# Performance work log

Measured on AMD Instinct MI355X. Metric: run time of the kernel, lower is better.

The kernel has to match this reference:

```python
import jax, jax.numpy as jnp
import numpy as np

N, D, H, C, E, I, L, B = 16000, 128, 2, 128, 256000, 512, 2, 64
NTYPES = 10


def setup_inputs() -> dict:
    key = jax.random.key(0)
    ks = jax.random.split(key, 20)
    s = 0.05
    inp = {
        'x': jax.random.normal(ks[0], (N, D), jnp.float32),
        'hetro_emb': jax.random.normal(ks[1], (NTYPES, D), jnp.float32) * s,
        'Wq': jax.random.normal(ks[2], (D, H * C), jnp.float32) * s,
        'bq': jnp.zeros((H * C,), jnp.float32),
        'Wk': jax.random.normal(ks[3], (D, H * C), jnp.float32) * s,
        'bk': jnp.zeros((H * C,), jnp.float32),
        'Wv': jax.random.normal(ks[4], (D, H * C), jnp.float32) * s,
        'bv': jnp.zeros((H * C,), jnp.float32),
        'We': jax.random.normal(ks[5], (D, H * C), jnp.float32) * s,
        'Wskip': jax.random.normal(ks[6], (D, C), jnp.float32) * s,
        'bskip': jnp.zeros((C,), jnp.float32),
        'ln_gamma': jnp.ones((L, D), jnp.float32),
        'ln_beta': jnp.zeros((L, D), jnp.float32),
        'ffn_w1': jax.random.normal(ks[7], (L, D, I), jnp.float32) * s,
        'ffn_b1': jnp.zeros((L, I), jnp.float32),
        'ffn_w2': jax.random.normal(ks[8], (L, I, D), jnp.float32) * s,
        'ffn_b2': jnp.zeros((L, D), jnp.float32),
        'edge_index': jax.random.randint(ks[9], (2, E), 0, N, jnp.int64),
        'edge_type': jax.random.randint(ks[10], (E,), 0, NTYPES, jnp.int64),
        'mask_idx': jax.random.randint(ks[11], (B,), 0, N, jnp.int64),
    }
    return inp


def _layer_norm(h, gamma, beta, eps=1e-6):
    mu = h.mean(-1, keepdims=True)
    var = ((h - mu) ** 2).mean(-1, keepdims=True)
    return (h - mu) * jax.lax.rsqrt(var + eps) * gamma + beta


def reference(x, hetro_emb, Wq, bq, Wk, bk, Wv, bv, We, Wskip, bskip,
              ln_gamma, ln_beta, ffn_w1, ffn_b1, ffn_w2, ffn_b2,
              edge_index, edge_type, mask_idx):
    src, dst = edge_index[0], edge_index[1]  # messages flow src(j) -> dst(i)
    edge_attr_raw = hetro_emb[edge_type]     # [E, D], computed once outside the layer loop
    scale = 1.0 / jnp.sqrt(jnp.asarray(C, x.dtype))

    h = x
    pre = h
    for l in range(L):
        # shared GRANConv weights across layers (same module appended n_gcn_layer times)
        q = (h @ Wq + bq).reshape(-1, H, C)
        k = (h @ Wk + bk).reshape(-1, H, C)
        v = (h @ Wv + bv).reshape(-1, H, C)
        eproj = (edge_attr_raw @ We).reshape(-1, H, C)  # [E, H, C]
        kj = k[src] + eproj                              # [E, H, C]
        logits = (q[dst] * kj).sum(-1) * scale           # [E, H]
        # segment softmax over destination nodes
        m = jax.ops.segment_max(logits, dst, num_segments=N)  # [N, H]
        a = jnp.exp(logits - m[dst])
        ssum = jax.ops.segment_sum(a, dst, num_segments=N)
        alpha = a / (ssum[dst] + 1e-16)                  # [E, H]
        msg = (v[src] + eproj) * alpha[..., None]        # [E, H, C]
        agg = jax.ops.segment_sum(msg, dst, num_segments=N)  # [N, H, C]
        out = agg.mean(1) + (h @ Wskip + bskip)          # concat=False -> head mean; root skip
        # residual + LN + FFN (no activation between the two FFN linears)
        hres = out + pre
        hln = _layer_norm(hres, ln_gamma[l], ln_beta[l])
        h = (hln @ ffn_w1[l] + ffn_b1[l]) @ ffn_w2[l] + ffn_b2[l]
        pre = h

    return h[mask_idx]  # [B, D]
```

## Files before the change

kernel.cpp:

```cpp
#include <hip/hip_runtime.h>
#include <hip/hip_bf16.h>
#include <math.h>

#define DD 128
#define QW 896
#define CAP 128
#define NB 125
#define BCAP 4096

typedef _Float16 f16x8 __attribute__((ext_vector_type(8)));
typedef _Float16 f16x2 __attribute__((ext_vector_type(2)));
typedef float f32x4 __attribute__((ext_vector_type(4)));

__device__ __forceinline__ float fdot2f(f16x2 a, f16x2 b, float c) {
#if __has_builtin(__builtin_amdgcn_fdot2)
  return __builtin_amdgcn_fdot2(a, b, c, false);
#else
  return fmaf((float)a[0], (float)b[0], fmaf((float)a[1], (float)b[1], c));
#endif
}

__global__ __launch_bounds__(256) void csr_count(const int* __restrict__ edst,
                                                 int* __restrict__ bcnt, int E) {
  __shared__ int h[NB];
  const int tid = threadIdx.x;
  if (tid < NB) h[tid] = 0;
  __syncthreads();
  const int e0 = blockIdx.x * 2048;
  for (int k = 0; k < 8; ++k) {
    int e = e0 + k * 256 + tid;
    if (e < E) atomicAdd(&h[edst[e] >> 7], 1);
  }
  __syncthreads();
  if (tid < NB && h[tid]) atomicAdd(&bcnt[tid], h[tid]);
}

__global__ __launch_bounds__(128) void csr_scan(const int* __restrict__ bcnt,
                                                int* __restrict__ bbase,
                                                int* __restrict__ bcursor,
                                                int* __restrict__ offs, int E, int Nn) {
  __shared__ int sc[128];
  const int tid = threadIdx.x;
  sc[tid] = (tid < NB) ? bcnt[tid] : 0;
  __syncthreads();
  for (int d = 1; d < 128; d <<= 1) {
    int t = (tid >= d) ? sc[tid - d] : 0;
    __syncthreads();
    sc[tid] += t;
    __syncthreads();
  }
  const int excl = tid ? sc[tid - 1] : 0;
  if (tid < NB) { bbase[tid] = excl; bcursor[tid] = excl; }
  if (tid == 0) { bbase[NB] = E; offs[Nn] = E; }
}

__global__ __launch_bounds__(256) void csr_scatter(const int* __restrict__ edst,
                                                   const int* __restrict__ esrc,
                                                   const int* __restrict__ etyp,
                                                   int* __restrict__ bcursor,
                                                   unsigned* __restrict__ ebuf, int E) {
  __shared__ int h[NB], cur[NB];
  const int tid = threadIdx.x;
  if (tid < NB) h[tid] = 0;
  __syncthreads();
  const int e0 = blockIdx.x * 2048;
  int dd[8];
  for (int k = 0; k < 8; ++k) {
    int e = e0 + k * 256 + tid;
    dd[k] = (e < E) ? edst[e] : -1;
    if (dd[k] >= 0) atomicAdd(&h[dd[k] >> 7], 1);
  }
  __syncthreads();
  if (tid < NB && h[tid]) cur[tid] = atomicAdd(&bcursor[tid], h[tid]);
  __syncthreads();
  for (int k = 0; k < 8; ++k) {
    int e = e0 + k * 256 + tid;
    if (dd[k] >= 0) {
      int pos = atomicAdd(&cur[dd[k] >> 7], 1);
      ebuf[pos] = (unsigned)esrc[e] | ((unsigned)etyp[e] << 14) |
                  ((unsigned)(dd[k] & 127) << 18);
    }
  }
}

__global__ __launch_bounds__(256) void csr_fine(const unsigned* __restrict__ ebuf,
                                                const int* __restrict__ bbase,
                                                unsigned* __restrict__ epk,
                                                int* __restrict__ offs,
                                                int* __restrict__ dcnt) {
  __shared__ unsigned sed[BCAP];
  __shared__ unsigned sout[BCAP];
  __shared__ int fh[128], sc[128], fc[128], hb[64];
  const int b = blockIdx.x, tid = threadIdx.x;
  const int base = bbase[b], cnt = bbase[b + 1] - base;
  for (int idx = tid; idx < cnt; idx += 256) sed[idx] = ebuf[base + idx];
  if (tid < 128) fh[tid] = 0;
  if (tid < 64) hb[tid] = 0;
  __syncthreads();
  for (int idx = tid; idx < cnt; idx += 256) atomicAdd(&fh[(sed[idx] >> 18) & 127], 1);
  __syncthreads();
  if (tid < 128) sc[tid] = fh[tid];
  __syncthreads();
  for (int d = 1; d < 128; d <<= 1) {
    int t = (tid < 128 && tid >= d) ? sc[tid - d] : 0;
    __syncthreads();
    if (tid < 128) sc[tid] += t;
    __syncthreads();
  }
  if (tid < 128) {
    const int excl = tid ? sc[tid - 1] : 0;
    offs[b * 128 + tid] = base + excl;
    fc[tid] = excl;
    atomicAdd(&hb[min(fh[tid], 63)], 1);
  }
  __syncthreads();
  if (tid < 64 && hb[tid]) atomicAdd(&dcnt[tid], hb[tid]);
  for (int idx = tid; idx < cnt; idx += 256) {
    const unsigned v = sed[idx];
    const int pos = atomicAdd(&fc[(v >> 18) & 127], 1);
    sout[pos] = (v & 0x3FFF) | (((v >> 14) & 0xF) << 18);
  }
  __syncthreads();
  for (int idx = tid; idx < cnt; idx += 256) epk[base + idx] = sout[idx];
}

__global__ __launch_bounds__(64) void deg_scan(const int* __restrict__ dcnt,
                                               int* __restrict__ dcur) {
  const int t = threadIdx.x;
  int s = 0;
  for (int d = t + 1; d < 64; ++d) s += dcnt[d];
  dcur[t] = s;
}

__global__ __launch_bounds__(256) void deg_order(const int* __restrict__ offs,
                                                 int* __restrict__ dcur,
                                                 int* __restrict__ order, int Nn) {
  __shared__ int h[64], cbase[64];
  const int tid = threadIdx.x;
  const int i = blockIdx.x * 256 + tid;
  if (tid < 64) h[tid] = 0;
  __syncthreads();
  int bk = -1;
  if (i < Nn) {
    bk = min(offs[i + 1] - offs[i], 63);
    atomicAdd(&h[bk], 1);
  }
  __syncthreads();
  if (tid < 64) {
    const int c = h[tid];
    cbase[tid] = c ? atomicAdd(&dcur[tid], c) : 0;
    h[tid] = 0;
  }
  __syncthreads();
  if (bk >= 0) {
    const int pos = cbase[bk] + atomicAdd(&h[bk], 1);
    order[pos] = i;
  }
}

__global__ __launch_bounds__(256) void pp_cast(
    const float* __restrict__ Wq, const float* __restrict__ Wk,
    const float* __restrict__ Wv, const float* __restrict__ Wsk,
    const float* __restrict__ bq, const float* __restrict__ bk,
    const float* __restrict__ bv, const float* __restrict__ bsk,
    const float* __restrict__ hemb, const float* __restrict__ We,
    const float* __restrict__ x,
    const float* __restrict__ fw1, const float* __restrict__ fb1,
    const float* __restrict__ fw2, const float* __restrict__ fb2,
    _Float16* __restrict__ WcatT, float* __restrict__ Wcat, float* __restrict__ bcat,
    _Float16* __restrict__ epth, _Float16* __restrict__ xh,
    _Float16* __restrict__ fw1h,
    float* __restrict__ bfv, float* __restrict__ bzero, int Nn) {
  int t = blockIdx.x * 256 + threadIdx.x;
  if (t < 256) {
    int l = t >> 7, j = t & 127;
    const float* b1 = fb1 + l * 512;
    const float* w2 = fw2 + (size_t)l * 65536 + j;
    float s0 = fb2[l * 128 + j], s1 = 0.f, s2 = 0.f, s3 = 0.f;
    for (int k = 0; k < 512; k += 4) {
      s0 = fmaf(b1[k], w2[(size_t)k * 128], s0);
      s1 = fmaf(b1[k + 1], w2[(size_t)(k + 1) * 128], s1);
      s2 = fmaf(b1[k + 2], w2[(size_t)(k + 2) * 128], s2);
      s3 = fmaf(b1[k + 3], w2[(size_t)(k + 3) * 128], s3);
    }
    bfv[t] = ((s0 + s1) + (s2 + s3));
    return;
  }
  t -= 256;
  if (t < 2560) {
    int ty = t >> 8, col = t & 255;
    float s0 = 0.f, s1 = 0.f, s2 = 0.f, s3 = 0.f;
    const float* hr = hemb + ty * 128;
    for (int c = 0; c < 128; c += 4) {
      s0 = fmaf(hr[c], We[c * 256 + col], s0);
      s1 = fmaf(hr[c + 1], We[(c + 1) * 256 + col], s1);
      s2 = fmaf(hr[c + 2], We[(c + 2) * 256 + col], s2);
      s3 = fmaf(hr[c + 3], We[(c + 3) * 256 + col], s3);
    }
    epth[t] = (_Float16)((s0 + s1) + (s2 + s3));
    return;
  }
  t -= 2560;
  if (t < 114688) {
    int n = t >> 7, k = t & 127;
    float v;
    if (n < 256) v = Wq[k * 256 + n];
    else if (n < 512) v = Wk[k * 256 + (n - 256)];
    else if (n < 768) v = Wv[k * 256 + (n - 512)];
    else v = Wsk[k * 128 + (n - 768)];
    WcatT[t] = (_Float16)v;
    Wcat[k * 896 + n] = v;
    return;
  }
  t -= 114688;
  if (t < 896) {
    float v;
    if (t < 256) v = bq[t];
    else if (t < 512) v = bk[t - 256];
    else if (t < 768) v = bv[t - 512];
    else v = bsk[t - 768];
    bcat[t] = v;
    return;
  }
  t -= 896;
  if (t < 1024) { bzero[t] = 0.f; return; }
  t -= 1024;
  if (t < 16384) {
    float4 v0 = *reinterpret_cast<const float4*>(fw1 + (size_t)t * 8);
    float4 v1 = *reinterpret_cast<const float4*>(fw1 + (size_t)t * 8 + 4);
    f16x8 o;
    o[0] = (_Float16)v0.x; o[1] = (_Float16)v0.y; o[2] = (_Float16)v0.z; o[3] = (_Float16)v0.w;
    o[4] = (_Float16)v1.x; o[5] = (_Float16)v1.y; o[6] = (_Float16)v1.z; o[7] = (_Float16)v1.w;
    *reinterpret_cast<f16x8*>(fw1h + (size_t)t * 8) = o;
    return;
  }
  t -= 16384;
  if (t < Nn * 16) {
    float4 v0 = *reinterpret_cast<const float4*>(x + (size_t)t * 8);
    float4 v1 = *reinterpret_cast<const float4*>(x + (size_t)t * 8 + 4);
    f16x8 o;
    o[0] = (_Float16)v0.x; o[1] = (_Float16)v0.y; o[2] = (_Float16)v0.z; o[3] = (_Float16)v0.w;
    o[4] = (_Float16)v1.x; o[5] = (_Float16)v1.y; o[6] = (_Float16)v1.z; o[7] = (_Float16)v1.w;
    *reinterpret_cast<f16x8*>(xh + (size_t)t * 8) = o;
  }
}

__global__ __launch_bounds__(256) void tr_fw2(const float* __restrict__ fw2,
                                              _Float16* __restrict__ fw2Th) {
  __shared__ _Float16 tile[64][65];
  const int l = blockIdx.z;
  const int k0 = blockIdx.x * 64, j0 = blockIdx.y * 64;
  const size_t base = (size_t)l * 65536;
  const int tid = threadIdx.x;
  for (int idx = tid; idx < 4096; idx += 256) {
    int r = idx >> 6, c = idx & 63;
    tile[r][c] = (_Float16)fw2[base + (size_t)(k0 + r) * 128 + j0 + c];
  }
  __syncthreads();
  for (int idx = tid; idx < 4096; idx += 256) {
    int r = idx >> 6, c = idx & 63;
    fw2Th[base + (size_t)(j0 + r) * 512 + k0 + c] = tile[c][r];
  }
}

__global__ __launch_bounds__(256) void pp_bmid(const float* __restrict__ bfv,
                                               const float* __restrict__ Wcat,
                                               const float* __restrict__ bcat,
                                               float* __restrict__ bmid) {
  int t = blockIdx.x * 256 + threadIdx.x;
  if (t >= 1024) return;
  if (t < 128) { bmid[t] = bfv[t]; return; }
  int n = t - 128;
  float s0 = bcat[n], s1 = 0.f, s2 = 0.f, s3 = 0.f;
  for (int c = 0; c < 128; c += 4) {
    s0 = fmaf(bfv[c], Wcat[c * 896 + n], s0);
    s1 = fmaf(bfv[c + 1], Wcat[(c + 1) * 896 + n], s1);
    s2 = fmaf(bfv[c + 2], Wcat[(c + 2) * 896 + n], s2);
    s3 = fmaf(bfv[c + 3], Wcat[(c + 3) * 896 + n], s3);
  }
  bmid[t] = ((s0 + s1) + (s2 + s3));
}

__global__ __launch_bounds__(256) void wf_gemm(const _Float16* __restrict__ fw1h,
                                               const _Float16* __restrict__ fw2Th,
                                               float* __restrict__ Wf,
                                               _Float16* __restrict__ Wfh,
                                               _Float16* __restrict__ BtMid0) {
  const int z = blockIdx.z;
  const _Float16* A = fw1h + z * 65536;
  const _Float16* Bt = fw2Th + z * 65536;
  const int tid = threadIdx.x;
  const int wid = tid >> 6, lane = tid & 63;
  const int wr = wid >> 1, wc = wid & 1;
  const int il = lane & 15, g = lane >> 4;
  const int row0 = wr * 64, col0 = wc * 64;
  const _Float16* Ap = A + (size_t)(row0 + il) * 512 + 8 * g;
  const _Float16* Bp = Bt + (size_t)(col0 + il) * 512 + 8 * g;
  f32x4 acc[4][4];
#pragma unroll
  for (int a = 0; a < 4; ++a)
#pragma unroll
    for (int b = 0; b < 4; ++b) acc[a][b] = (f32x4){0.f, 0.f, 0.f, 0.f};
  for (int k0 = 0; k0 < 512; k0 += 32) {
    f16x8 af[4], bf[4];
#pragma unroll
    for (int f = 0; f < 4; ++f) {
      af[f] = *reinterpret_cast<const f16x8*>(Ap + (size_t)(f * 16) * 512 + k0);
      bf[f] = *reinterpret_cast<const f16x8*>(Bp + (size_t)(f * 16) * 512 + k0);
    }
#pragma unroll
    for (int fi = 0; fi < 4; ++fi)
#pragma unroll
      for (int fj = 0; fj < 4; ++fj)
        acc[fi][fj] = __builtin_amdgcn_mfma_f32_16x16x32_f16(af[fi], bf[fj], acc[fi][fj], 0, 0, 0);
  }
#pragma unroll
  for (int fj = 0; fj < 4; ++fj) {
    const int col = col0 + fj * 16 + il;
#pragma unroll
    for (int fi = 0; fi < 4; ++fi) {
#pragma unroll
      for (int i = 0; i < 4; ++i) {
        const int row = row0 + fi * 16 + g * 4 + i;
        const float v = acc[fi][fj][i];
        Wf[z * 16384 + row * 128 + col] = v;
        if (z == 0) {
          Wfh[row * 128 + col] = (_Float16)v;
          BtMid0[col * 128 + row] = (_Float16)v;
        }
      }
    }
  }
}

template <bool HAS_CFH, bool HAS_CH, bool HAS_CHT>
__global__ __launch_bounds__(256) void gemm_tn_f16(const _Float16* __restrict__ A,
                                                   const _Float16* __restrict__ Bt,
                                                   const float* __restrict__ bias,
                                                   _Float16* __restrict__ Cfh, int NF,
                                                   _Float16* __restrict__ Ch, int choff, int ldh,
                                                   _Float16* __restrict__ ChT, int ldt,
                                                   int M, int N, int K) {
  const int tid = threadIdx.x;
  const int wid = tid >> 6, lane = tid & 63;
  const int wr = wid >> 1, wc = wid & 1;
  const int il = lane & 15, g = lane >> 4;
  const int row0 = blockIdx.y * 128 + wr * 64;
  const int col0 = blockIdx.x * 128 + wc * 64;
  const _Float16* Ap = A + (size_t)(row0 + il) * K + 8 * g;
  const _Float16* Bp = Bt + (size_t)(col0 + il) * K + 8 * g;
  f32x4 acc[4][4];
#pragma unroll
  for (int a = 0; a < 4; ++a)
#pragma unroll
    for (int b = 0; b < 4; ++b) acc[a][b] = (f32x4){0.f, 0.f, 0.f, 0.f};
  for (int k0 = 0; k0 < K; k0 += 32) {
    f16x8 af[4], bf[4];
#pragma unroll
    for (int f = 0; f < 4; ++f) {
      af[f] = *reinterpret_cast<const f16x8*>(Ap + (size_t)(f * 16) * K + k0);
      bf[f] = *reinterpret_cast<const f16x8*>(Bp + (size_t)(f * 16) * K + k0);
    }
#pragma unroll
    for (int fi = 0; fi < 4; ++fi)
#pragma unroll
      for (int fj = 0; fj < 4; ++fj)
        acc[fi][fj] = __builtin_amdgcn_mfma_f32_16x16x32_f16(af[fi], bf[fj], acc[fi][fj], 0, 0, 0);
  }
#pragma unroll
  for (int fj = 0; fj < 4; ++fj) {
    const int col = col0 + fj * 16 + il;
    const float b = bias[col];
#pragma unroll
    for (int fi = 0; fi < 4; ++fi) {
#pragma unroll
      for (int i = 0; i < 4; ++i) {
        const int row = row0 + fi * 16 + g * 4 + i;
        const float v = acc[fi][fj][i] + b;
        if constexpr (HAS_CFH) { if (col < NF) Cfh[(size_t)row * NF + col] = (_Float16)v; }
        if constexpr (HAS_CH) { if (col >= choff) Ch[(size_t)row * ldh + (col - choff)] = (_Float16)v; }
        if constexpr (HAS_CHT) { ChT[(size_t)col * ldt + row] = (_Float16)v; }
      }
    }
  }
}

__global__ __launch_bounds__(256) void node_attn_ln_kernel(
    const _Float16* __restrict__ QKVSh, const _Float16* __restrict__ epth,
    const _Float16* __restrict__ hpre,
    const int* __restrict__ offs, const unsigned* __restrict__ epk,
    const int* __restrict__ order,
    const float* __restrict__ gamma, const float* __restrict__ beta,
    _Float16* __restrict__ hlnh, int Nn) {
  __shared__ float sl0[4][CAP], sl1[4][CAP];
  __shared__ unsigned spk[4][CAP];
  __shared__ float sqe[4][2][10];
  __shared__ __align__(16) _Float16 elds[2560];
  const int tid = threadIdx.x;
  for (int t = tid; t < 1280; t += 256)
    reinterpret_cast<unsigned*>(elds)[t] = reinterpret_cast<const unsigned*>(epth)[t];
  __syncthreads();
  const int w = tid >> 6, lane = tid & 63;
  const int i = order[blockIdx.x * 4 + w];
  const int sub = lane >> 5;
  const int r = lane & 31;
  const int half = r >> 4;
  const int co = r << 3;
  const float scale = 0.08838834764831845f;
  f16x8 qh = *reinterpret_cast<const f16x8*>(QKVSh + (size_t)i * QW + co);
  const f16x2* q2 = reinterpret_cast<const f16x2*>(&qh);
#pragma unroll
  for (int ty = 0; ty < 10; ++ty) {
    f16x8 ev = *reinterpret_cast<const f16x8*>(elds + (ty << 8) + co);
    const f16x2* e2 = reinterpret_cast<const f16x2*>(&ev);
    float s = 0.f;
#pragma unroll
    for (int p2 = 0; p2 < 4; ++p2) s = fdot2f(q2[p2], e2[p2], s);
    s += __shfl_xor(s, 1); s += __shfl_xor(s, 2);
    s += __shfl_xor(s, 4); s += __shfl_xor(s, 8);
    if (lane < 32 && (r & 15) == 0) sqe[w][half][ty] = s * scale;
  }
  __threadfence_block();
  float m_me = -1e30f, s_me = 0.f;
  float acc[8] = {0.f};
  const int ebeg = offs[i], eend = offs[i + 1];
  for (int cs = ebeg; cs < eend; cs += CAP) {
    const int cnt = min(CAP, eend - cs);
    const int last = cnt - 1;
    for (int j = lane; j < cnt; j += 64) spk[w][j] = epk[cs + j];
    __threadfence_block();
    float cmax = -1e30f;
    {
      unsigned pk0 = spk[w][min(sub, last)];
      unsigned pk1 = spk[w][min(2 + sub, last)];
      f16x8 kv0 = *reinterpret_cast<const f16x8*>(QKVSh + (size_t)(pk0 & 0x3FFFF) * QW + 256 + co);
      f16x8 kv1 = *reinterpret_cast<const f16x8*>(QKVSh + (size_t)(pk1 & 0x3FFFF) * QW + 256 + co);
      int ty0 = pk0 >> 18, ty1 = pk1 >> 18;
      for (int j = 0; j < cnt; j += 2) {
        f16x8 kc = kv0;
        const int tyc = ty0;
        kv0 = kv1; ty0 = ty1;
        unsigned pkn = spk[w][min(j + 4 + sub, last)];
        ty1 = pkn >> 18;
        kv1 = *reinterpret_cast<const f16x8*>(QKVSh + (size_t)(pkn & 0x3FFFF) * QW + 256 + co);
        const f16x2* k2 = reinterpret_cast<const f16x2*>(&kc);
        float d = 0.f;
#pragma unroll
        for (int p2 = 0; p2 < 4; ++p2) d = fdot2f(q2[p2], k2[p2], d);
        d += __shfl_xor(d, 1); d += __shfl_xor(d, 2);
        d += __shfl_xor(d, 4); d += __shfl_xor(d, 8);
        d = d * scale + sqe[w][half][tyc];
        if (j + sub < cnt) {
          cmax = fmaxf(cmax, d);
          if ((r & 15) == 0) (half ? sl1 : sl0)[w][j + sub] = d;
        }
      }
    }
    cmax = fmaxf(cmax, __shfl_xor(cmax, 32));
    const float nm = fmaxf(m_me, cmax);
    const float rr = __expf(m_me - nm);
    s_me *= rr;
#pragma unroll
    for (int t = 0; t < 8; ++t) acc[t] *= rr;
    m_me = nm;
    __threadfence_block();
    {
      unsigned pk0 = spk[w][min(sub, last)];
      unsigned pk1 = spk[w][min(2 + sub, last)];
      f16x8 vv0 = *reinterpret_cast<const f16x8*>(QKVSh + (size_t)(pk0 & 0x3FFFF) * QW + 512 + co);
      f16x8 ee0 = *reinterpret_cast<const f16x8*>(elds + ((pk0 >> 18) << 8) + co);
      f16x8 vv1 = *reinterpret_cast<const f16x8*>(QKVSh + (size_t)(pk1 & 0x3FFFF) * QW + 512 + co);
      f16x8 ee1 = *reinterpret_cast<const f16x8*>(elds + ((pk1 >> 18) << 8) + co);
      const float* slme = (half ? sl1 : sl0)[w];
      float ls = 0.f;
      for (int j = 0; j < cnt; j += 2) {
        f16x8 vc = vv0, ec = ee0;
        vv0 = vv1; ee0 = ee1;
        unsigned pkn = spk[w][min(j + 4 + sub, last)];
        vv1 = *reinterpret_cast<const f16x8*>(QKVSh + (size_t)(pkn & 0x3FFFF) * QW + 512 + co);
        ee1 = *reinterpret_cast<const f16x8*>(elds + ((pkn >> 18) << 8) + co);
        const int jc = j + sub;
        float e = 0.f;
        if (jc < cnt) e = __expf(slme[jc] - m_me);
        ls += e;
#pragma unroll
        for (int t = 0; t < 8; ++t) acc[t] = fmaf((float)vc[t] + (float)ec[t], e, acc[t]);
      }
      s_me += ls;
    }
  }
  const float s_tot = s_me + __shfl_xor(s_me, 32);
  const float invme = 1.f / (s_tot + 1e-16f);
  float g[8];
#pragma unroll
  for (int t = 0; t < 8; ++t) {
    float a = acc[t] + __shfl_xor(acc[t], 32);
    a *= invme;
    g[t] = 0.5f * (a + __shfl_xor(a, 16));
  }
  const int cm = (r & 15) << 3;
  f16x8 sk = *reinterpret_cast<const f16x8*>(QKVSh + (size_t)i * QW + 768 + cm);
  f16x8 pr = *reinterpret_cast<const f16x8*>(hpre + (size_t)i * DD + cm);
  float xv[8];
#pragma unroll
  for (int t = 0; t < 8; ++t) xv[t] = g[t] + (float)sk[t] + (float)pr[t];
  float sm = 0.f;
#pragma unroll
  for (int t = 0; t < 8; ++t) sm += xv[t];
  sm += __shfl_xor(sm, 1); sm += __shfl_xor(sm, 2);
  sm += __shfl_xor(sm, 4); sm += __shfl_xor(sm, 8);
  const float mu = sm * (1.f / 128.f);
  float dx[8], vvs = 0.f;
#pragma unroll
  for (int t = 0; t < 8; ++t) { dx[t] = xv[t] - mu; vvs += dx[t] * dx[t]; }
  vvs += __shfl_xor(vvs, 1); vvs += __shfl_xor(vvs, 2);
  vvs += __shfl_xor(vvs, 4); vvs += __shfl_xor(vvs, 8);
  const float rstd = rsqrtf(vvs * (1.f / 128.f) + 1e-6f);
  if (lane < 16) {
    float4 gm0 = *reinterpret_cast<const float4*>(gamma + cm);
    float4 gm1 = *reinterpret_cast<const float4*>(gamma + cm + 4);
    float4 bt0 = *reinterpret_cast<const float4*>(beta + cm);
    float4 bt1 = *reinterpret_cast<const float4*>(beta + cm + 4);
    f16x8 o;
    o[0] = (_Float16)(dx[0] * rstd * gm0.x + bt0.x);
    o[1] = (_Float16)(dx[1] * rstd * gm0.y + bt0.y);
    o[2] = (_Float16)(dx[2] * rstd * gm0.z + bt0.z);
    o[3] = (_Float16)(dx[3] * rstd * gm0.w + bt0.w);
    o[4] = (_Float16)(dx[4] * rstd * gm1.x + bt1.x);
    o[5] = (_Float16)(dx[5] * rstd * gm1.y + bt1.y);
    o[6] = (_Float16)(dx[6] * rstd * gm1.z + bt1.z);
    o[7] = (_Float16)(dx[7] * rstd * gm1.w + bt1.w);
    *reinterpret_cast<f16x8*>(hlnh + (size_t)i * DD + cm) = o;
  }
}

__global__ __launch_bounds__(128) void final_kernel(const _Float16* __restrict__ hlnh1,
                                                    const float* __restrict__ Wf,
                                                    const float* __restrict__ bfv,
                                                    const int* __restrict__ midx,
                                                    float* __restrict__ out) {
  __shared__ float rowv[128];
  const int b = blockIdx.x, j = threadIdx.x;
  const int row = midx[b];
  rowv[j] = (float)hlnh1[(size_t)row * DD + j];
  __syncthreads();
  const float* w1 = Wf + 16384 + j;
  float s = bfv[128 + j];
#pragma unroll 4
  for (int c = 0; c < 128; ++c) s = fmaf(rowv[c], w1[c * 128], s);
  out[b * DD + j] = s;
}

extern "C" void kernel_launch(void* const* d_in, const int* in_sizes, int n_in,
                              void* d_out, int out_size, void* d_ws, size_t ws_size,
                              hipStream_t stream) {
  const float* x    = (const float*)d_in[0];
  const float* hemb = (const float*)d_in[1];
  const float* Wq   = (const float*)d_in[2];
  const float* bq   = (const float*)d_in[3];
  const float* Wk   = (const float*)d_in[4];
  const float* bk   = (const float*)d_in[5];
  const float* Wv   = (const float*)d_in[6];
  const float* bv   = (const float*)d_in[7];
  const float* We   = (const float*)d_in[8];
  const float* Wsk  = (const float*)d_in[9];
  const float* bsk  = (const float*)d_in[10];
  const float* lng  = (const float*)d_in[11];
  const float* lnb  = (const float*)d_in[12];
  const float* fw1  = (const float*)d_in[13];
  const float* fb1  = (const float*)d_in[14];
  const float* fw2  = (const float*)d_in[15];
  const float* fb2  = (const float*)d_in[16];
  const int* eidx   = (const int*)d_in[17];
  const int* etyp   = (const int*)d_in[18];
  const int* midx   = (const int*)d_in[19];

  const int Nn = in_sizes[0] / DD;
  const int E = in_sizes[18];

  const int* esrc = eidx;
  const int* edst = eidx + E;

  char* p = (char*)d_ws;
  auto alloc = [&](size_t bytes) -> void* {
    void* r = (void*)p;
    p += (bytes + 255) & ~(size_t)255;
    return r;
  };
  _Float16* QKVSh = (_Float16*)alloc((size_t)Nn * QW * 2);
  _Float16* xh    = (_Float16*)alloc((size_t)Nn * DD * 2);
  _Float16* hln0  = (_Float16*)alloc((size_t)Nn * DD * 2);
  _Float16* hln1  = (_Float16*)alloc((size_t)Nn * DD * 2);
  _Float16* h1h   = (_Float16*)alloc((size_t)Nn * DD * 2);
  _Float16* WcatT = (_Float16*)alloc((size_t)QW * DD * 2);
  float*    Wcat  = (float*)alloc((size_t)DD * QW * 4);
  float*    bcat  = (float*)alloc(QW * 4);
  _Float16* epth  = (_Float16*)alloc(2560 * 2);
  _Float16* fw1h  = (_Float16*)alloc((size_t)2 * DD * 512 * 2);
  _Float16* fw2Th = (_Float16*)alloc((size_t)2 * DD * 512 * 2);
  float*    Wf    = (float*)alloc(2 * 128 * 128 * 4);
  _Float16* Wfh   = (_Float16*)alloc(128 * 128 * 2);
  float*    bfv   = (float*)alloc(256 * 4);
  float*    bzero = (float*)alloc(1024 * 4);
  _Float16* BtMid = (_Float16*)alloc((size_t)1024 * 128 * 2);
  float*    bmid  = (float*)alloc(1024 * 4);
  int* offs   = (int*)alloc((size_t)(Nn + 1) * 4);
  int* bcnt   = (int*)alloc((NB + 1) * 4);
  int* bbase  = (int*)alloc((NB + 1) * 4);
  int* bcursor= (int*)alloc((NB + 1) * 4);
  int* dcnt   = (int*)alloc(64 * 4);
  int* dcur   = (int*)alloc(64 * 4);
  int* order  = (int*)alloc((size_t)Nn * 4);
  unsigned* ebuf = (unsigned*)alloc((size_t)E * 4);
  unsigned* epk  = (unsigned*)alloc((size_t)E * 4);

  hipMemsetAsync(bcnt, 0, (NB + 1) * sizeof(int), stream);
  hipMemsetAsync(dcnt, 0, 64 * sizeof(int), stream);
  csr_count<<<(E + 2047) / 2048, 256, 0, stream>>>(edst, bcnt, E);
  csr_scan<<<1, 128, 0, stream>>>(bcnt, bbase, bcursor, offs, E, Nn);
  csr_scatter<<<(E + 2047) / 2048, 256, 0, stream>>>(edst, esrc, etyp, bcursor, ebuf, E);
  csr_fine<<<NB, 256, 0, stream>>>(ebuf, bbase, epk, offs, dcnt);
  deg_scan<<<1, 64, 0, stream>>>(dcnt, dcur);
  deg_order<<<(Nn + 255) / 256, 256, 0, stream>>>(offs, dcur, order, Nn);

  const int pc_threads = 256 + 2560 + 114688 + 896 + 1024 + 16384 + Nn * 16;
  pp_cast<<<(pc_threads + 255) / 256, 256, 0, stream>>>(
      Wq, Wk, Wv, Wsk, bq, bk, bv, bsk, hemb, We, x, fw1, fb1, fw2, fb2,
      WcatT, Wcat, bcat, epth, xh, fw1h, bfv, bzero, Nn);
  tr_fw2<<<dim3(8, 2, 2), 256, 0, stream>>>(fw2, fw2Th);
  pp_bmid<<<4, 256, 0, stream>>>(bfv, Wcat, bcat, bmid);
  wf_gemm<<<dim3(1, 1, 2), 256, 0, stream>>>(fw1h, fw2Th, Wf, Wfh, BtMid);
  gemm_tn_f16<false, false, true><<<dim3(7, 1), 256, 0, stream>>>(
      Wfh, WcatT, bzero, nullptr, 0, nullptr, 0, 0, BtMid + 16384, 128, 128, 896, 128);

  gemm_tn_f16<false, true, false><<<dim3(QW / 128, Nn / 128), 256, 0, stream>>>(
      xh, WcatT, bcat, nullptr, 0, QKVSh, 0, QW, nullptr, 0, Nn, QW, DD);
  node_attn_ln_kernel<<<Nn / 4, 256, 0, stream>>>(QKVSh, epth, xh, offs, epk, order,
                                                  lng, lnb, hln0, Nn);
  gemm_tn_f16<true, true, false><<<dim3(1024 / 128, Nn / 128), 256, 0, stream>>>(
      hln0, BtMid, bmid, h1h, 128, QKVSh, 128, QW, nullptr, 0, Nn, 1024, DD);
  node_attn_ln_kernel<<<Nn / 4, 256, 0, stream>>>(QKVSh, epth, h1h, offs, epk, order,
                                                  lng + DD, lnb + DD, hln1, Nn);
  final_kernel<<<64, 128, 0, stream>>>(hln1, Wf, bfv, midx, (float*)d_out);
}
```

Baseline: 257.4 us.

## Fold q·edge-embedding terms and attention scale into projection GEMM columns

Adds 20 extra output columns to the QKV projection that hold q·eproj for every head and edge type. They are computed by folding Wq·eproj into the weight matrix, and the 1/sqrt(C) scale is folded into Wq and bq. The attention kernel then reads these precomputed values instead of doing per-node dot products against the 10 type embeddings. It also replaces the global atomic histograms in CSR building with per-block partial arrays, which removes two memsets. The fw2 transpose is merged into the pp_cast launch. In exchange the GEMMs are wider (896→1024 and 1024→1152 columns), the QKV buffer row stride grows, and the q·e term now carries fp16 rounding.

```diff
diff --git a/kernel.cpp b/kernel.cpp
--- a/kernel.cpp
+++ b/kernel.cpp
@@ -3,7 +3,7 @@
 #include <math.h>
 
 #define DD 128
-#define QW 896
+#define QW2 1024
 #define CAP 128
 #define NB 125
 #define BCAP 4096
@@ -21,7 +21,7 @@
 }
 
 __global__ __launch_bounds__(256) void csr_count(const int* __restrict__ edst,
-                                                 int* __restrict__ bcnt, int E) {
+                                                 int* __restrict__ bparts, int E) {
   __shared__ int h[NB];
   const int tid = threadIdx.x;
   if (tid < NB) h[tid] = 0;
@@ -32,16 +32,18 @@
     if (e < E) atomicAdd(&h[edst[e] >> 7], 1);
   }
   __syncthreads();
-  if (tid < NB && h[tid]) atomicAdd(&bcnt[tid], h[tid]);
-}
-
-__global__ __launch_bounds__(128) void csr_scan(const int* __restrict__ bcnt,
+  if (tid < 128) bparts[blockIdx.x * 128 + tid] = (tid < NB) ? h[tid] : 0;
+}
+
+__global__ __launch_bounds__(128) void csr_scan(const int* __restrict__ bparts, int nblk,
                                                 int* __restrict__ bbase,
                                                 int* __restrict__ bcursor,
                                                 int* __restrict__ offs, int E, int Nn) {
   __shared__ int sc[128];
   const int tid = threadIdx.x;
-  sc[tid] = (tid < NB) ? bcnt[tid] : 0;
+  int s = 0;
+  for (int b = 0; b < nblk; ++b) s += bparts[b * 128 + tid];
+  sc[tid] = (tid < NB) ? s : 0;
   __syncthreads();
   for (int d = 1; d < 128; d <<= 1) {
     int t = (tid >= d) ? sc[tid - d] : 0;
@@ -87,7 +89,7 @@
                                                 const int* __restrict__ bbase,
                                                 unsigned* __restrict__ epk,
                                                 int* __restrict__ offs,
-                                                int* __restrict__ dcnt) {
+                                                int* __restrict__ dparts) {
   __shared__ unsigned sed[BCAP];
   __shared__ unsigned sout[BCAP];
   __shared__ int fh[128], sc[128], fc[128], hb[64];
@@ -114,7 +116,7 @@
     atomicAdd(&hb[min(fh[tid], 63)], 1);
   }
   __syncthreads();
-  if (tid < 64 && hb[tid]) atomicAdd(&dcnt[tid], hb[tid]);
+  if (tid < 64) dparts[b * 64 + tid] = hb[tid];
   for (int idx = tid; idx < cnt; idx += 256) {
     const unsigned v = sed[idx];
     const int pos = atomicAdd(&fc[(v >> 18) & 127], 1);
@@ -124,12 +126,17 @@
   for (int idx = tid; idx < cnt; idx += 256) epk[base + idx] = sout[idx];
 }
 
-__global__ __launch_bounds__(64) void deg_scan(const int* __restrict__ dcnt,
+__global__ __launch_bounds__(64) void deg_scan(const int* __restrict__ dparts, int nblk,
                                                int* __restrict__ dcur) {
+  __shared__ int tot[64];
   const int t = threadIdx.x;
   int s = 0;
-  for (int d = t + 1; d < 64; ++d) s += dcnt[d];
-  dcur[t] = s;
+  for (int b = 0; b < nblk; ++b) s += dparts[b * 64 + t];
+  tot[t] = s;
+  __syncthreads();
+  int acc = 0;
+  for (int d = t + 1; d < 64; ++d) acc += tot[d];
+  dcur[t] = acc;
 }
 
 __global__ __launch_bounds__(256) void deg_order(const int* __restrict__ offs,
@@ -168,9 +175,28 @@
     const float* __restrict__ fw1, const float* __restrict__ fb1,
     const float* __restrict__ fw2, const float* __restrict__ fb2,
     _Float16* __restrict__ WcatT, float* __restrict__ Wcat, float* __restrict__ bcat,
-    _Float16* __restrict__ epth, _Float16* __restrict__ xh,
-    _Float16* __restrict__ fw1h,
-    float* __restrict__ bfv, float* __restrict__ bzero, int Nn) {
+    _Float16* __restrict__ epth, float* __restrict__ eptf, _Float16* __restrict__ xh,
+    _Float16* __restrict__ fw1h, _Float16* __restrict__ fw2Th,
+    float* __restrict__ bfv, float* __restrict__ bzero, int Nn, int nb0) {
+  __shared__ _Float16 tile[64][65];
+  const float scale = 0.08838834764831845f;
+  if (blockIdx.x >= nb0) {
+    const int tb = blockIdx.x - nb0;
+    const int l = tb >> 4, r2 = tb & 15;
+    const int k0 = (r2 >> 1) << 6, j0 = (r2 & 1) << 6;
+    const size_t base = (size_t)l * 65536;
+    const int tid = threadIdx.x;
+    for (int idx = tid; idx < 4096; idx += 256) {
+      int rr = idx >> 6, cc = idx & 63;
+      tile[rr][cc] = (_Float16)fw2[base + (size_t)(k0 + rr) * 128 + j0 + cc];
+    }
+    __syncthreads();
+    for (int idx = tid; idx < 4096; idx += 256) {
+      int rr = idx >> 6, cc = idx & 63;
+      fw2Th[base + (size_t)(j0 + rr) * 512 + k0 + cc] = tile[cc][rr];
+    }
+    return;
+  }
   int t = blockIdx.x * 256 + threadIdx.x;
   if (t < 256) {
     int l = t >> 7, j = t & 127;
@@ -197,32 +223,36 @@
       s2 = fmaf(hr[c + 2], We[(c + 2) * 256 + col], s2);
       s3 = fmaf(hr[c + 3], We[(c + 3) * 256 + col], s3);
     }
-    epth[t] = (_Float16)((s0 + s1) + (s2 + s3));
+    const float v = ((s0 + s1) + (s2 + s3));
+    epth[t] = (_Float16)v;
+    eptf[t] = v;
     return;
   }
   t -= 2560;
-  if (t < 114688) {
+  if (t < 131072) {
     int n = t >> 7, k = t & 127;
     float v;
-    if (n < 256) v = Wq[k * 256 + n];
+    if (n < 256) v = scale * Wq[k * 256 + n];
     else if (n < 512) v = Wk[k * 256 + (n - 256)];
     else if (n < 768) v = Wv[k * 256 + (n - 512)];
-    else v = Wsk[k * 128 + (n - 768)];
+    else if (n < 896) v = Wsk[k * 128 + (n - 768)];
+    else v = 0.f;
     WcatT[t] = (_Float16)v;
-    Wcat[k * 896 + n] = v;
+    Wcat[k * 1024 + n] = v;
     return;
   }
-  t -= 114688;
-  if (t < 896) {
+  t -= 131072;
+  if (t < 1024) {
     float v;
-    if (t < 256) v = bq[t];
+    if (t < 256) v = scale * bq[t];
     else if (t < 512) v = bk[t - 256];
     else if (t < 768) v = bv[t - 512];
-    else v = bsk[t - 768];
+    else if (t < 896) v = bsk[t - 768];
+    else v = 0.f;
     bcat[t] = v;
     return;
   }
-  t -= 896;
+  t -= 1024;
   if (t < 1024) { bzero[t] = 0.f; return; }
   t -= 1024;
   if (t < 16384) {
@@ -245,21 +275,35 @@
   }
 }
 
-__global__ __launch_bounds__(256) void tr_fw2(const float* __restrict__ fw2,
-                                              _Float16* __restrict__ fw2Th) {
-  __shared__ _Float16 tile[64][65];
-  const int l = blockIdx.z;
-  const int k0 = blockIdx.x * 64, j0 = blockIdx.y * 64;
-  const size_t base = (size_t)l * 65536;
-  const int tid = threadIdx.x;
-  for (int idx = tid; idx < 4096; idx += 256) {
-    int r = idx >> 6, c = idx & 63;
-    tile[r][c] = (_Float16)fw2[base + (size_t)(k0 + r) * 128 + j0 + c];
-  }
-  __syncthreads();
-  for (int idx = tid; idx < 4096; idx += 256) {
-    int r = idx >> 6, c = idx & 63;
-    fw2Th[base + (size_t)(j0 + r) * 512 + k0 + c] = tile[c][r];
+__global__ __launch_bounds__(256) void eq_cols(float* __restrict__ Wcat,
+                                               const float* __restrict__ eptf,
+                                               float* __restrict__ bcat,
+                                               _Float16* __restrict__ WcatT) {
+  int t = blockIdx.x * 256 + threadIdx.x;
+  if (t < 2560) {
+    const int n = t >> 7, k = t & 127;
+    const int h = n / 10, ty = n % 10;
+    const float* wrow = Wcat + (size_t)k * 1024 + h * 128;
+    const float* ep = eptf + ty * 256 + h * 128;
+    float s0 = 0.f, s1 = 0.f, s2 = 0.f, s3 = 0.f;
+    for (int c = 0; c < 128; c += 4) {
+      s0 = fmaf(wrow[c], ep[c], s0);
+      s1 = fmaf(wrow[c + 1], ep[c + 1], s1);
+      s2 = fmaf(wrow[c + 2], ep[c + 2], s2);
+      s3 = fmaf(wrow[c + 3], ep[c + 3], s3);
+    }
+    const float v = ((s0 + s1) + (s2 + s3));
+    WcatT[(size_t)(896 + n) * 128 + k] = (_Float16)v;
+    Wcat[(size_t)k * 1024 + 896 + n] = v;
+    return;
+  }
+  t -= 2560;
+  if (t < 20) {
+    const int h = t / 10, ty = t % 10;
+    const float* ep = eptf + ty * 256 + h * 128;
+    float s = 0.f;
+    for (int c = 0; c < 128; ++c) s = fmaf(bcat[h * 128 + c], ep[c], s);
+    bcat[896 + t] = s;
   }
 }
 
@@ -268,15 +312,15 @@
                                                const float* __restrict__ bcat,
                                                float* __restrict__ bmid) {
   int t = blockIdx.x * 256 + threadIdx.x;
-  if (t >= 1024) return;
+  if (t >= 1152) return;
   if (t < 128) { bmid[t] = bfv[t]; return; }
   int n = t - 128;
   float s0 = bcat[n], s1 = 0.f, s2 = 0.f, s3 = 0.f;
   for (int c = 0; c < 128; c += 4) {
-    s0 = fmaf(bfv[c], Wcat[c * 896 + n], s0);
-    s1 = fmaf(bfv[c + 1], Wcat[(c + 1) * 896 + n], s1);
-    s2 = fmaf(bfv[c + 2], Wcat[(c + 2) * 896 + n], s2);
-    s3 = fmaf(bfv[c + 3], Wcat[(c + 3) * 896 + n], s3);
+    s0 = fmaf(bfv[c], Wcat[c * 1024 + n], s0);
+    s1 = fmaf(bfv[c + 1], Wcat[(c + 1) * 1024 + n], s1);
+    s2 = fmaf(bfv[c + 2], Wcat[(c + 2) * 1024 + n], s2);
+    s3 = fmaf(bfv[c + 3], Wcat[(c + 3) * 1024 + n], s3);
   }
   bmid[t] = ((s0 + s1) + (s2 + s3));
 }
@@ -406,20 +450,10 @@
   const int r = lane & 31;
   const int half = r >> 4;
   const int co = r << 3;
-  const float scale = 0.08838834764831845f;
-  f16x8 qh = *reinterpret_cast<const f16x8*>(QKVSh + (size_t)i * QW + co);
+  f16x8 qh = *reinterpret_cast<const f16x8*>(QKVSh + (size_t)i * QW2 + co);
   const f16x2* q2 = reinterpret_cast<const f16x2*>(&qh);
-#pragma unroll
-  for (int ty = 0; ty < 10; ++ty) {
-    f16x8 ev = *reinterpret_cast<const f16x8*>(elds + (ty << 8) + co);
-    const f16x2* e2 = reinterpret_cast<const f16x2*>(&ev);
-    float s = 0.f;
-#pragma unroll
-    for (int p2 = 0; p2 < 4; ++p2) s = fdot2f(q2[p2], e2[p2], s);
-    s += __shfl_xor(s, 1); s += __shfl_xor(s, 2);
-    s += __shfl_xor(s, 4); s += __shfl_xor(s, 8);
-    if (lane < 32 && (r & 15) == 0) sqe[w][half][ty] = s * scale;
-  }
+  if (lane < 20)
+    sqe[w][lane / 10][lane % 10] = (float)QKVSh[(size_t)i * QW2 + 896 + lane];
   __threadfence_block();
   float m_me = -1e30f, s_me = 0.f;
   float acc[8] = {0.f};
@@ -433,8 +467,8 @@
     {
       unsigned pk0 = spk[w][min(sub, last)];
       unsigned pk1 = spk[w][min(2 + sub, last)];
-      f16x8 kv0 = *reinterpret_cast<const f16x8*>(QKVSh + (size_t)(pk0 & 0x3FFFF) * QW + 256 + co);
-      f16x8 kv1 = *reinterpret_cast<const f16x8*>(QKVSh + (size_t)(pk1 & 0x3FFFF) * QW + 256 + co);
+      f16x8 kv0 = *reinterpret_cast<const f16x8*>(QKVSh + (size_t)(pk0 & 0x3FFFF) * QW2 + 256 + co);
+      f16x8 kv1 = *reinterpret_cast<const f16x8*>(QKVSh + (size_t)(pk1 & 0x3FFFF) * QW2 + 256 + co);
       int ty0 = pk0 >> 18, ty1 = pk1 >> 18;
       for (int j = 0; j < cnt; j += 2) {
         f16x8 kc = kv0;
@@ -442,14 +476,14 @@
         kv0 = kv1; ty0 = ty1;
         unsigned pkn = spk[w][min(j + 4 + sub, last)];
         ty1 = pkn >> 18;
-        kv1 = *reinterpret_cast<const f16x8*>(QKVSh + (size_t)(pkn & 0x3FFFF) * QW + 256 + co);
+        kv1 = *reinterpret_cast<const f16x8*>(QKVSh + (size_t)(pkn & 0x3FFFF) * QW2 + 256 + co);
         const f16x2* k2 = reinterpret_cast<const f16x2*>(&kc);
         float d = 0.f;
 #pragma unroll
         for (int p2 = 0; p2 < 4; ++p2) d = fdot2f(q2[p2], k2[p2], d);
         d += __shfl_xor(d, 1); d += __shfl_xor(d, 2);
         d += __shfl_xor(d, 4); d += __shfl_xor(d, 8);
-        d = d * scale + sqe[w][half][tyc];
+        d += sqe[w][half][tyc];
         if (j + sub < cnt) {
           cmax = fmaxf(cmax, d);
           if ((r & 15) == 0) (half ? sl1 : sl0)[w][j + sub] = d;
@@ -467,9 +501,9 @@
     {
       unsigned pk0 = spk[w][min(sub, last)];
       unsigned pk1 = spk[w][min(2 + sub, last)];
-      f16x8 vv0 = *reinterpret_cast<const f16x8*>(QKVSh + (size_t)(pk0 & 0x3FFFF) * QW + 512 + co);
+      f16x8 vv0 = *reinterpret_cast<const f16x8*>(QKVSh + (size_t)(pk0 & 0x3FFFF) * QW2 + 512 + co);
       f16x8 ee0 = *reinterpret_cast<const f16x8*>(elds + ((pk0 >> 18) << 8) + co);
-      f16x8 vv1 = *reinterpret_cast<const f16x8*>(QKVSh + (size_t)(pk1 & 0x3FFFF) * QW + 512 + co);
+      f16x8 vv1 = *reinterpret_cast<const f16x8*>(QKVSh + (size_t)(pk1 & 0x3FFFF) * QW2 + 512 + co);
       f16x8 ee1 = *reinterpret_cast<const f16x8*>(elds + ((pk1 >> 18) << 8) + co);
       const float* slme = (half ? sl1 : sl0)[w];
       float ls = 0.f;
@@ -477,7 +511,7 @@
         f16x8 vc = vv0, ec = ee0;
         vv0 = vv1; ee0 = ee1;
         unsigned pkn = spk[w][min(j + 4 + sub, last)];
-        vv1 = *reinterpret_cast<const f16x8*>(QKVSh + (size_t)(pkn & 0x3FFFF) * QW + 512 + co);
+        vv1 = *reinterpret_cast<const f16x8*>(QKVSh + (size_t)(pkn & 0x3FFFF) * QW2 + 512 + co);
         ee1 = *reinterpret_cast<const f16x8*>(elds + ((pkn >> 18) << 8) + co);
         const int jc = j + sub;
         float e = 0.f;
@@ -499,7 +533,7 @@
     g[t] = 0.5f * (a + __shfl_xor(a, 16));
   }
   const int cm = (r & 15) << 3;
-  f16x8 sk = *reinterpret_cast<const f16x8*>(QKVSh + (size_t)i * QW + 768 + cm);
+  f16x8 sk = *reinterpret_cast<const f16x8*>(QKVSh + (size_t)i * QW2 + 768 + cm);
   f16x8 pr = *reinterpret_cast<const f16x8*>(hpre + (size_t)i * DD + cm);
   float xv[8];
 #pragma unroll
@@ -587,58 +621,59 @@
     p += (bytes + 255) & ~(size_t)255;
     return r;
   };
-  _Float16* QKVSh = (_Float16*)alloc((size_t)Nn * QW * 2);
+  _Float16* QKVSh = (_Float16*)alloc((size_t)Nn * QW2 * 2);
   _Float16* xh    = (_Float16*)alloc((size_t)Nn * DD * 2);
   _Float16* hln0  = (_Float16*)alloc((size_t)Nn * DD * 2);
   _Float16* hln1  = (_Float16*)alloc((size_t)Nn * DD * 2);
   _Float16* h1h   = (_Float16*)alloc((size_t)Nn * DD * 2);
-  _Float16* WcatT = (_Float16*)alloc((size_t)QW * DD * 2);
-  float*    Wcat  = (float*)alloc((size_t)DD * QW * 4);
-  float*    bcat  = (float*)alloc(QW * 4);
+  _Float16* WcatT = (_Float16*)alloc((size_t)1024 * DD * 2);
+  float*    Wcat  = (float*)alloc((size_t)DD * 1024 * 4);
+  float*    bcat  = (float*)alloc(1024 * 4);
   _Float16* epth  = (_Float16*)alloc(2560 * 2);
+  float*    eptf  = (float*)alloc(2560 * 4);
   _Float16* fw1h  = (_Float16*)alloc((size_t)2 * DD * 512 * 2);
   _Float16* fw2Th = (_Float16*)alloc((size_t)2 * DD * 512 * 2);
   float*    Wf    = (float*)alloc(2 * 128 * 128 * 4);
   _Float16* Wfh   = (_Float16*)alloc(128 * 128 * 2);
   float*    bfv   = (float*)alloc(256 * 4);
   float*    bzero = (float*)alloc(1024 * 4);
-  _Float16* BtMid = (_Float16*)alloc((size_t)1024 * 128 * 2);
-  float*    bmid  = (float*)alloc(1024 * 4);
+  _Float16* BtMid = (_Float16*)alloc((size_t)1152 * 128 * 2);
+  float*    bmid  = (float*)alloc(1152 * 4);
   int* offs   = (int*)alloc((size_t)(Nn + 1) * 4);
-  int* bcnt   = (int*)alloc((NB + 1) * 4);
   int* bbase  = (int*)alloc((NB + 1) * 4);
   int* bcursor= (int*)alloc((NB + 1) * 4);
-  int* dcnt   = (int*)alloc(64 * 4);
   int* dcur   = (int*)alloc(64 * 4);
   int* order  = (int*)alloc((size_t)Nn * 4);
+  const int nsblk = (E + 2047) / 2048;
+  int* bparts = (int*)alloc((size_t)nsblk * 128 * 4);
+  int* dparts = (int*)alloc((size_t)NB * 64 * 4);
   unsigned* ebuf = (unsigned*)alloc((size_t)E * 4);
   unsigned* epk  = (unsigned*)alloc((size_t)E * 4);
 
-  hipMemsetAsync(bcnt, 0, (NB + 1) * sizeof(int), stream);
-  hipMemsetAsync(dcnt, 0, 64 * sizeof(int), stream);
-  csr_count<<<(E + 2047) / 2048, 256, 0, stream>>>(edst, bcnt, E);
-  csr_scan<<<1, 128, 0, stream>>>(bcnt, bbase, bcursor, offs, E, Nn);
-  csr_scatter<<<(E + 2047) / 2048, 256, 0, stream>>>(edst, esrc, etyp, bcursor, ebuf, E);
-  csr_fine<<<NB, 256, 0, stream>>>(ebuf, bbase, epk, offs, dcnt);
-  deg_scan<<<1, 64, 0, stream>>>(dcnt, dcur);
+  csr_count<<<nsblk, 256, 0, stream>>>(edst, bparts, E);
+  csr_scan<<<1, 128, 0, stream>>>(bparts, nsblk, bbase, bcursor, offs, E, Nn);
+  csr_scatter<<<nsblk, 256, 0, stream>>>(edst, esrc, etyp, bcursor, ebuf, E);
+  csr_fine<<<NB, 256, 0, stream>>>(ebuf, bbase, epk, offs, dparts);
+  deg_scan<<<1, 64, 0, stream>>>(dparts, NB, dcur);
   deg_order<<<(Nn + 255) / 256, 256, 0, stream>>>(offs, dcur, order, Nn);
 
-  const int pc_threads = 256 + 2560 + 114688 + 896 + 1024 + 16384 + Nn * 16;
-  pp_cast<<<(pc_threads + 255) / 256, 256, 0, stream>>>(
+  const int pc_threads = 256 + 2560 + 131072 + 1024 + 1024 + 16384 + Nn * 16;
+  const int nb0 = (pc_threads + 255) / 256;
+  pp_cast<<<nb0 + 32, 256, 0, stream>>>(
       Wq, Wk, Wv, Wsk, bq, bk, bv, bsk, hemb, We, x, fw1, fb1, fw2, fb2,
-      WcatT, Wcat, bcat, epth, xh, fw1h, bfv, bzero, Nn);
-  tr_fw2<<<dim3(8, 2, 2), 256, 0, stream>>>(fw2, fw2Th);
-  pp_bmid<<<4, 256, 0, stream>>>(bfv, Wcat, bcat, bmid);
+      WcatT, Wcat, bcat, epth, eptf, xh, fw1h, fw2Th, bfv, bzero, Nn, nb0);
+  eq_cols<<<11, 256, 0, stream>>>(Wcat, eptf, bcat, WcatT);
   wf_gemm<<<dim3(1, 1, 2), 256, 0, stream>>>(fw1h, fw2Th, Wf, Wfh, BtMid);
-  gemm_tn_f16<false, false, true><<<dim3(7, 1), 256, 0, stream>>>(
-      Wfh, WcatT, bzero, nullptr, 0, nullptr, 0, 0, BtMid + 16384, 128, 128, 896, 128);
-
-  gemm_tn_f16<false, true, false><<<dim3(QW / 128, Nn / 128), 256, 0, stream>>>(
-      xh, WcatT, bcat, nullptr, 0, QKVSh, 0, QW, nullptr, 0, Nn, QW, DD);
+  pp_bmid<<<5, 256, 0, stream>>>(bfv, Wcat, bcat, bmid);
+  gemm_tn_f16<false, false, true><<<dim3(8, 1), 256, 0, stream>>>(
+      Wfh, WcatT, bzero, nullptr, 0, nullptr, 0, 0, BtMid + 16384, 128, 128, 1024, 128);
+
+  gemm_tn_f16<false, true, false><<<dim3(1024 / 128, Nn / 128), 256, 0, stream>>>(
+      xh, WcatT, bcat, nullptr, 0, QKVSh, 0, QW2, nullptr, 0, Nn, 1024, DD);
   node_attn_ln_kernel<<<Nn / 4, 256, 0, stream>>>(QKVSh, epth, xh, offs, epk, order,
                                                   lng, lnb, hln0, Nn);
-  gemm_tn_f16<true, true, false><<<dim3(1024 / 128, Nn / 128), 256, 0, stream>>>(
-      hln0, BtMid, bmid, h1h, 128, QKVSh, 128, QW, nullptr, 0, Nn, 1024, DD);
+  gemm_tn_f16<true, true, false><<<dim3(1152 / 128, Nn / 128), 256, 0, stream>>>(
+      hln0, BtMid, bmid, h1h, 128, QKVSh, 128, QW2, nullptr, 0, Nn, 1152, DD);
   node_attn_ln_kernel<<<Nn / 4, 256, 0, stream>>>(QKVSh, epth, h1h, offs, epk, order,
                                                   lng + DD, lnb + DD, hln1, Nn);
   final_kernel<<<64, 128, 0, stream>>>(hln1, Wf, bfv, midx, (float*)d_out);
```

Result: slower. 281.9 us (+9.5%).
